# Performance work log

Hardware: AMD Instinct MI355X
Metric: run time of the kernel (lower is better)

The kernel has to match this reference:

```python
import jax, jax.numpy as jnp
import numpy as np

N_NODES = 10000
N_EDGES = 50000
UNITS = 64
NUM_GAUSSIANS = 50
MIN_D, MAX_D, GAMMA = 0.0, 30.0, 10.0


def setup_inputs() -> dict:
    key = jax.random.key(0)
    ks = jax.random.split(key, 8)
    node_features = jax.random.normal(ks[0], (N_NODES, UNITS), dtype=jnp.float32)
    edge_indices = jax.random.randint(ks[1], (2, N_EDGES), 0, N_NODES, dtype=jnp.int32)
    distances = jax.random.uniform(ks[2], (N_EDGES,), dtype=jnp.float32) * MAX_D
    # filter network params (Dense(units) -> Dense(units*units)), glorot-ish scales
    W1 = jax.random.normal(ks[3], (NUM_GAUSSIANS, UNITS), dtype=jnp.float32) * 0.13
    b1 = jnp.zeros((UNITS,), dtype=jnp.float32)
    W2 = jax.random.normal(ks[4], (UNITS, UNITS * UNITS), dtype=jnp.float32) * 0.02
    b2 = jnp.zeros((UNITS * UNITS,), dtype=jnp.float32)
    # transform Dense(units, use_bias=False)
    Wt = jax.random.normal(ks[5], (UNITS, UNITS), dtype=jnp.float32) * 0.125
    return {"node_features": node_features, "edge_indices": edge_indices,
            "distances": distances, "W1": W1, "b1": b1, "W2": W2, "b2": b2, "Wt": Wt}


def reference(node_features, edge_indices, distances, W1, b1, W2, b2, Wt):
    # Gaussian basis expansion: [E, G]
    centers = jnp.linspace(MIN_D, MAX_D, NUM_GAUSSIANS, dtype=jnp.float32)
    dist_feat = jnp.exp(-GAMMA * jnp.square(distances[:, None] - centers[None, :]))
    # filter-generating network -> per-edge [E, U, U] filters
    h = dist_feat @ W1 + b1
    filters = (h @ W2 + b2).reshape(-1, UNITS, UNITS)
    # gather source node feats, linear transform, per-edge matvec
    src = node_features[edge_indices[0]]            # [E, U]
    transformed = src @ Wt                          # [E, U]
    filtered = jnp.einsum('eij,ej->ei', filters, transformed)  # [E, U]
    # scatter-sum to destination nodes
    messages = jax.ops.segment_sum(filtered, edge_indices[1], num_segments=N_NODES)
    # shifted softplus: f(0) = 0
    return jax.nn.softplus(messages) - jnp.log(jnp.float32(2.0))
```

## Files before the change

### kernel.cpp

```cpp
#include <hip/hip_runtime.h>
#include <stdint.h>

#define UNITS 64
#define UU 4096
#define NG 50
#define NSLOT 51
#define GAMMA_C 10.0f
#define STEP_C (30.0f / 49.0f)
#define NWIN 4
#define NBKT 47

typedef __attribute__((ext_vector_type(8))) short bf16x8;
typedef __attribute__((ext_vector_type(4))) float f32x4;

__device__ __forceinline__ float bfu(uint16_t v) { return __uint_as_float(((uint32_t)v) << 16); }
__device__ __forceinline__ uint16_t f2bf(float x) {
  uint32_t u = __float_as_uint(x);
  u += 0x7fffu + ((u >> 16) & 1u);
  return (uint16_t)(u >> 16);
}
__device__ __forceinline__ uint32_t pk_bf16(float lo, float hi) {
  uint32_t r;
  asm("v_cvt_pk_bf16_f32 %0, %1, %2" : "=v"(r) : "v"(lo), "v"(hi));
  return r;
}
__device__ __forceinline__ int lo_of(float d) {
  int lo = (int)floorf(d * (1.0f / STEP_C)) - 1;
  return min(max(lo, 0), NG - NWIN);
}

__global__ void __launch_bounds__(256) k_at(
    const float* __restrict__ W1, const float* __restrict__ b1,
    const float* __restrict__ W2, const float* __restrict__ b2,
    const float* __restrict__ Wt, const float* __restrict__ dist,
    uint16_t* __restrict__ T5B, float* __restrict__ msg,
    int* __restrict__ bins, int* __restrict__ eidx,
    int n_out, int E, int ne) {
  int g = blockIdx.y, bx = blockIdx.x;
  if (g >= NSLOT) {
    if (g < NSLOT + 8) {
      int n4 = n_out >> 2;
      float4 z = {0.f, 0.f, 0.f, 0.f};
      for (int t = ((g - NSLOT) * 16 + bx) * 256 + threadIdx.x; t < n4; t += 128 * 256)
        reinterpret_cast<float4*>(msg)[t] = z;
    } else {
      __shared__ int hloc[NBKT];
      for (int i = threadIdx.x; i < NBKT; i += 256) hloc[i] = 0;
      __syncthreads();
      int tt = bx * 256 + threadIdx.x;
      for (int e = tt; e < E; e += 4096)
        atomicAdd(&hloc[lo_of(dist[e])], 1);
      __syncthreads();
      for (int i = threadIdx.x; i < NBKT; i += 256)
        if (hloc[i]) atomicAdd(&bins[i], hloc[i]);
      for (int i = tt; i < ne; i += 4096) eidx[i] = -1;
    }
    return;
  }
  __shared__ float Aloc[256];
  __shared__ float WtL[64 * 65];
  const int t = threadIdx.x;
  const int ij = bx * 256 + t;

  #pragma unroll
  for (int q = 0; q < 4; ++q) {
    int idx = q * 256 + t;
    float4 v = reinterpret_cast<const float4*>(Wt)[idx];
    int mm = idx >> 4, jj = (idx & 15) * 4;
    float* dst = &WtL[mm * 65 + jj];
    dst[0] = v.x; dst[1] = v.y; dst[2] = v.z; dst[3] = v.w;
  }
  {
    float acc = 0.f;
    if (g < NG) {
      const float* w1r = W1 + g * UNITS;
      #pragma unroll 8
      for (int k = 0; k < UNITS; ++k) acc = fmaf(w1r[k], W2[k * UU + ij], acc);
    } else {
      #pragma unroll 8
      for (int k = 0; k < UNITS; ++k) acc = fmaf(b1[k], W2[k * UU + ij], acc);
      acc += b2[ij];
    }
    Aloc[t] = acc;
  }
  __syncthreads();

  const int i_local = t >> 6, m = t & 63;
  const float* ar = &Aloc[i_local * 64];
  const float* wr = &WtL[m * 65];
  float acc = 0.f;
  #pragma unroll 8
  for (int j = 0; j < UNITS; ++j) acc = fmaf(ar[j], wr[j], acc);
  const int gi = bx * 4 + i_local;
  T5B[(((g << 3) + (m >> 3)) << 9) + (gi << 3) + (m & 7)] = f2bf(acc);
}

__global__ void k_scan(const int* __restrict__ bins, int* __restrict__ base,
                       int* __restrict__ cursor) {
  int l = threadIdx.x;
  int v = (l < NBKT) ? ((bins[l] + 15) >> 4) << 4 : 0;
  int inc = v;
  #pragma unroll
  for (int s = 1; s < 64; s <<= 1) {
    int t = __shfl_up(inc, s, 64);
    if (l >= s) inc += t;
  }
  int exc = inc - v;
  if (l < NBKT) { base[l] = exc; cursor[l] = exc; }
  if (l == NBKT) base[NBKT] = exc;
}

__global__ void __launch_bounds__(256) k_scat(const float* __restrict__ dist,
                                              int* __restrict__ cursor,
                                              int* __restrict__ eidx, int E) {
  __shared__ int hcnt[NBKT], hbase[NBKT], hcur[NBKT];
  int per = (E + gridDim.x - 1) / gridDim.x;
  int e0 = blockIdx.x * per, e1 = min(e0 + per, E);
  for (int i = threadIdx.x; i < NBKT; i += 256) { hcnt[i] = 0; hcur[i] = 0; }
  __syncthreads();
  for (int e = e0 + threadIdx.x; e < e1; e += 256)
    atomicAdd(&hcnt[lo_of(dist[e])], 1);
  __syncthreads();
  for (int i = threadIdx.x; i < NBKT; i += 256)
    hbase[i] = hcnt[i] ? atomicAdd(&cursor[i], hcnt[i]) : 0;
  __syncthreads();
  for (int e = e0 + threadIdx.x; e < e1; e += 256) {
    int b = lo_of(dist[e]);
    int p = hbase[b] + atomicAdd(&hcur[b], 1);
    eidx[p] = e;
  }
}

__global__ void __launch_bounds__(256) k_em(
    const float* __restrict__ nf, const int* __restrict__ ei,
    const float* __restrict__ dist, const uint16_t* __restrict__ T5B,
    const int* __restrict__ eidx, const int* __restrict__ base,
    float* __restrict__ msg, int E) {
  __shared__ float tile[4][16 * 64];
  int w = threadIdx.x >> 6, l = threadIdx.x & 63;
  int lr = l & 15, lg = l >> 4;
  int t16 = (blockIdx.x * 4 + w) * 16;
  int total = base[NBKT];
  if (t16 >= total) return;

  int b = 0;
  #pragma unroll
  for (int i = 1; i < NBKT; ++i) b += (t16 >= base[i]);

  int e = eidx[t16 + lr];
  bool valid = (e >= 0);
  int src = valid ? ei[e] : 0;
  int dst = valid ? ei[E + e] : -1;
  float d = valid ? dist[e] : 3.0e30f;

  float df[5];
  #pragma unroll
  for (int s = 0; s < NWIN; ++s) {
    float tt = d - (float)(b + s) * STEP_C;
    df[s] = __expf(-GAMMA_C * tt * tt);
  }
  df[NWIN] = valid ? 1.f : 0.f;

  union { bf16x8 v; uint32_t u[4]; } afr[2];
  const float4* ab = reinterpret_cast<const float4*>(nf + src * UNITS) + lg * 2;
  #pragma unroll
  for (int kk = 0; kk < 2; ++kk) {
    float4 v0 = ab[kk * 8], v1 = ab[kk * 8 + 1];
    afr[kk].u[0] = pk_bf16(v0.x, v0.y);
    afr[kk].u[1] = pk_bf16(v0.z, v0.w);
    afr[kk].u[2] = pk_bf16(v1.x, v1.y);
    afr[kk].u[3] = pk_bf16(v1.z, v1.w);
  }

  f32x4 run[4] = {};
  #pragma unroll
  for (int s = 0; s < 5; ++s) {
    int g = (s < NWIN) ? (b + s) : NG;
    const char* bb = (const char*)T5B + (g << 13) + (lg << 10) + (lr << 6);
    f32x4 acc[4] = {};
    #pragma unroll
    for (int kk = 0; kk < 2; ++kk)
      #pragma unroll
      for (int nt = 0; nt < 4; ++nt) {
        bf16x8 bf = *reinterpret_cast<const bf16x8*>(bb + (kk << 12) + (nt << 4));
        acc[nt] = __builtin_amdgcn_mfma_f32_16x16x32_bf16(afr[kk].v, bf, acc[nt], 0, 0, 0);
      }
    float dfq[4];
    #pragma unroll
    for (int q = 0; q < 4; ++q) dfq[q] = __shfl(df[s], lg * 4 + q, 64);
    #pragma unroll
    for (int nt = 0; nt < 4; ++nt)
      #pragma unroll
      for (int q = 0; q < 4; ++q)
        run[nt][q] = fmaf(dfq[q], acc[nt][q], run[nt][q]);
  }

  float* tw = tile[w];
  #pragma unroll
  for (int q = 0; q < 4; ++q) {
    float4 v4 = {run[0][q], run[1][q], run[2][q], run[3][q]};
    *reinterpret_cast<float4*>(&tw[(lg * 4 + q) * 64 + 4 * lr]) = v4;
  }
  asm volatile("" ::: "memory");

  #pragma unroll
  for (int r = 0; r < 16; ++r) {
    int dr = __shfl(dst, r, 64);
    if (dr < 0) continue;
    atomicAdd(&msg[dr * UNITS + l], tw[r * 64 + l]);
  }
}

__global__ void k_final(const float* __restrict__ msg, float* __restrict__ out, int n) {
  int i = blockIdx.x * 256 + threadIdx.x;
  if (i >= n) return;
  float x = msg[i];
  float sp = (x > 0.f) ? (x + log1pf(__expf(-x))) : log1pf(__expf(x));
  out[i] = sp - 0.69314718056f;
}

extern "C" void kernel_launch(void* const* d_in, const int* in_sizes, int n_in,
                              void* d_out, int out_size, void* d_ws, size_t ws_size,
                              hipStream_t stream) {
  const float* nf   = (const float*)d_in[0];
  const int*   ei   = (const int*)d_in[1];
  const float* dist = (const float*)d_in[2];
  const float* W1   = (const float*)d_in[3];
  const float* b1   = (const float*)d_in[4];
  const float* W2   = (const float*)d_in[5];
  const float* b2   = (const float*)d_in[6];
  const float* Wt   = (const float*)d_in[7];
  float* out = (float*)d_out;

  int E = in_sizes[2];
  int n_out = out_size;

  int mt = E / 16 + NBKT + 1;
  int ne = mt * 16;

  char* ws = (char*)d_ws;
  size_t off_msg  = 417792;
  size_t off_bins = off_msg + (size_t)n_out * 4;
  size_t off_base = off_bins + 64 * 4;
  size_t off_cur  = off_base + 64 * 4;
  size_t off_eidx = off_cur + 64 * 4;

  uint16_t* T5B   = (uint16_t*)ws;
  float*    msg   = (float*)(ws + off_msg);
  int*      bins  = (int*)(ws + off_bins);
  int*      base  = (int*)(ws + off_base);
  int*      cursor= (int*)(ws + off_cur);
  int*      eidx  = (int*)(ws + off_eidx);

  hipMemsetAsync(bins, 0, 64 * 4, stream);

  k_at  <<<dim3(16, NSLOT + 9), 256, 0, stream>>>(W1, b1, W2, b2, Wt, dist,
                                                  T5B, msg, bins, eidx, n_out, E, ne);
  k_scan<<<1, 64, 0, stream>>>(bins, base, cursor);
  k_scat<<<64, 256, 0, stream>>>(dist, cursor, eidx, E);
  k_em  <<<(mt + 3) / 4, 256, 0, stream>>>(nf, ei, dist, T5B, eidx, base, msg, E);
  k_final<<<(n_out + 255) / 256, 256, 0, stream>>>(msg, out, n_out);
}
```

Measured before the change: 48.20 us.

## Restructure bucketing pipeline to fold scan and scatter into other kernels

Histogramming moves into its own small kernel that runs first. The per-block prefix scan and the bucket scatter are folded into extra blocks of k_at, and k_em recomputes tile bases from the bin counts with a wave scan and ballot. This removes the separate k_scan and k_scat launches. The final softplus kernel is also vectorised to float4. The cost is redundant scan work in every block and scatter blocks that compete with the filter-precompute blocks.

```diff
diff --git a/kernel.cpp b/kernel.cpp
--- a/kernel.cpp
+++ b/kernel.cpp
@@ -13,7 +13,6 @@
 typedef __attribute__((ext_vector_type(8))) short bf16x8;
 typedef __attribute__((ext_vector_type(4))) float f32x4;
 
-__device__ __forceinline__ float bfu(uint16_t v) { return __uint_as_float(((uint32_t)v) << 16); }
 __device__ __forceinline__ uint16_t f2bf(float x) {
   uint32_t u = __float_as_uint(x);
   u += 0x7fffu + ((u >> 16) & 1u);
@@ -27,6 +26,21 @@
 __device__ __forceinline__ int lo_of(float d) {
   int lo = (int)floorf(d * (1.0f / STEP_C)) - 1;
   return min(max(lo, 0), NG - NWIN);
+}
+
+__global__ void __launch_bounds__(256) k_hist(const float* __restrict__ dist,
+                                              int* __restrict__ bins,
+                                              int* __restrict__ eidx, int E, int ne) {
+  __shared__ int hloc[NBKT];
+  for (int i = threadIdx.x; i < NBKT; i += 256) hloc[i] = 0;
+  __syncthreads();
+  int tt = blockIdx.x * 256 + threadIdx.x;
+  for (int e = tt; e < E; e += 64 * 256)
+    atomicAdd(&hloc[lo_of(dist[e])], 1);
+  __syncthreads();
+  for (int i = threadIdx.x; i < NBKT; i += 256)
+    if (hloc[i]) atomicAdd(&bins[i], hloc[i]);
+  for (int i = tt; i < ne; i += 64 * 256) eidx[i] = -1;
 }
 
 __global__ void __launch_bounds__(256) k_at(
@@ -34,8 +48,8 @@
     const float* __restrict__ W2, const float* __restrict__ b2,
     const float* __restrict__ Wt, const float* __restrict__ dist,
     uint16_t* __restrict__ T5B, float* __restrict__ msg,
-    int* __restrict__ bins, int* __restrict__ eidx,
-    int n_out, int E, int ne) {
+    const int* __restrict__ bins, int* __restrict__ rsv, int* __restrict__ eidx,
+    int n_out, int E) {
   int g = blockIdx.y, bx = blockIdx.x;
   if (g >= NSLOT) {
     if (g < NSLOT + 8) {
@@ -43,17 +57,36 @@
       float4 z = {0.f, 0.f, 0.f, 0.f};
       for (int t = ((g - NSLOT) * 16 + bx) * 256 + threadIdx.x; t < n4; t += 128 * 256)
         reinterpret_cast<float4*>(msg)[t] = z;
-    } else {
-      __shared__ int hloc[NBKT];
-      for (int i = threadIdx.x; i < NBKT; i += 256) hloc[i] = 0;
-      __syncthreads();
-      int tt = bx * 256 + threadIdx.x;
-      for (int e = tt; e < E; e += 4096)
-        atomicAdd(&hloc[lo_of(dist[e])], 1);
-      __syncthreads();
-      for (int i = threadIdx.x; i < NBKT; i += 256)
-        if (hloc[i]) atomicAdd(&bins[i], hloc[i]);
-      for (int i = tt; i < ne; i += 4096) eidx[i] = -1;
+      return;
+    }
+    __shared__ int sbase[NBKT];
+    __shared__ int hcnt[NBKT], hbase[NBKT], hcur[NBKT];
+    int sb = (g - (NSLOT + 8)) * 16 + bx;
+    int per = (E + 63) >> 6;
+    int e0 = sb * per, e1 = min(e0 + per, E);
+    if (threadIdx.x < 64) {
+      int lane = threadIdx.x;
+      int cap = (lane < NBKT) ? ((bins[lane] + 15) & ~15) : 0;
+      int inc = cap;
+      #pragma unroll
+      for (int s = 1; s < 64; s <<= 1) {
+        int t = __shfl_up(inc, s, 64);
+        if (lane >= s) inc += t;
+      }
+      if (lane < NBKT) sbase[lane] = inc - cap;
+    }
+    for (int i = threadIdx.x; i < NBKT; i += 256) { hcnt[i] = 0; hcur[i] = 0; }
+    __syncthreads();
+    for (int e = e0 + threadIdx.x; e < e1; e += 256)
+      atomicAdd(&hcnt[lo_of(dist[e])], 1);
+    __syncthreads();
+    for (int i = threadIdx.x; i < NBKT; i += 256)
+      hbase[i] = hcnt[i] ? (sbase[i] + atomicAdd(&rsv[i], hcnt[i])) : 0;
+    __syncthreads();
+    for (int e = e0 + threadIdx.x; e < e1; e += 256) {
+      int b = lo_of(dist[e]);
+      int p = hbase[b] + atomicAdd(&hcur[b], 1);
+      eidx[p] = e;
     }
     return;
   }
@@ -95,59 +128,33 @@
   T5B[(((g << 3) + (m >> 3)) << 9) + (gi << 3) + (m & 7)] = f2bf(acc);
 }
 
-__global__ void k_scan(const int* __restrict__ bins, int* __restrict__ base,
-                       int* __restrict__ cursor) {
-  int l = threadIdx.x;
-  int v = (l < NBKT) ? ((bins[l] + 15) >> 4) << 4 : 0;
-  int inc = v;
-  #pragma unroll
-  for (int s = 1; s < 64; s <<= 1) {
-    int t = __shfl_up(inc, s, 64);
-    if (l >= s) inc += t;
-  }
-  int exc = inc - v;
-  if (l < NBKT) { base[l] = exc; cursor[l] = exc; }
-  if (l == NBKT) base[NBKT] = exc;
-}
-
-__global__ void __launch_bounds__(256) k_scat(const float* __restrict__ dist,
-                                              int* __restrict__ cursor,
-                                              int* __restrict__ eidx, int E) {
-  __shared__ int hcnt[NBKT], hbase[NBKT], hcur[NBKT];
-  int per = (E + gridDim.x - 1) / gridDim.x;
-  int e0 = blockIdx.x * per, e1 = min(e0 + per, E);
-  for (int i = threadIdx.x; i < NBKT; i += 256) { hcnt[i] = 0; hcur[i] = 0; }
-  __syncthreads();
-  for (int e = e0 + threadIdx.x; e < e1; e += 256)
-    atomicAdd(&hcnt[lo_of(dist[e])], 1);
-  __syncthreads();
-  for (int i = threadIdx.x; i < NBKT; i += 256)
-    hbase[i] = hcnt[i] ? atomicAdd(&cursor[i], hcnt[i]) : 0;
-  __syncthreads();
-  for (int e = e0 + threadIdx.x; e < e1; e += 256) {
-    int b = lo_of(dist[e]);
-    int p = hbase[b] + atomicAdd(&hcur[b], 1);
-    eidx[p] = e;
-  }
-}
-
 __global__ void __launch_bounds__(256) k_em(
     const float* __restrict__ nf, const int* __restrict__ ei,
     const float* __restrict__ dist, const uint16_t* __restrict__ T5B,
-    const int* __restrict__ eidx, const int* __restrict__ base,
+    const int* __restrict__ eidx, const int* __restrict__ bins,
     float* __restrict__ msg, int E) {
   __shared__ float tile[4][16 * 64];
   int w = threadIdx.x >> 6, l = threadIdx.x & 63;
   int lr = l & 15, lg = l >> 4;
-  int t16 = (blockIdx.x * 4 + w) * 16;
-  int total = base[NBKT];
-  if (t16 >= total) return;
-
-  int b = 0;
-  #pragma unroll
-  for (int i = 1; i < NBKT; ++i) b += (t16 >= base[i]);
-
-  int e = eidx[t16 + lr];
+  int tileW = blockIdx.x * 4 + w;
+
+  int c = (l < NBKT) ? bins[l] : 0;
+  int tcap = (c + 15) >> 4;
+  int p = tcap;
+  #pragma unroll
+  for (int s = 1; s < 64; s <<= 1) {
+    int tt = __shfl_up(p, s, 64);
+    if (l >= s) p += tt;
+  }
+  int total = __shfl(p, 63);
+  if (tileW >= total) return;
+
+  uint64_t mb = __ballot(tileW < p);
+  int b = __ffsll((unsigned long long)mb) - 1;
+  int pb = __shfl(p, b), tb = __shfl(tcap, b);
+  int lt = tileW - (pb - tb);
+
+  int e = eidx[(pb - tb + lt) * 16 + lr];
   bool valid = (e >= 0);
   int src = valid ? ei[e] : 0;
   int dst = valid ? ei[E + e] : -1;
@@ -211,12 +218,17 @@
   }
 }
 
-__global__ void k_final(const float* __restrict__ msg, float* __restrict__ out, int n) {
-  int i = blockIdx.x * 256 + threadIdx.x;
-  if (i >= n) return;
-  float x = msg[i];
-  float sp = (x > 0.f) ? (x + log1pf(__expf(-x))) : log1pf(__expf(x));
-  out[i] = sp - 0.69314718056f;
+__global__ void k_final(const float* __restrict__ msg, float* __restrict__ out,
+                        int n_out) {
+  int i4 = blockIdx.x * 256 + threadIdx.x;
+  if (i4 >= (n_out >> 2)) return;
+  float4 a = reinterpret_cast<const float4*>(msg)[i4];
+  float4 r;
+  r.x = ((a.x > 0.f) ? (a.x + log1pf(__expf(-a.x))) : log1pf(__expf(a.x))) - 0.69314718056f;
+  r.y = ((a.y > 0.f) ? (a.y + log1pf(__expf(-a.y))) : log1pf(__expf(a.y))) - 0.69314718056f;
+  r.z = ((a.z > 0.f) ? (a.z + log1pf(__expf(-a.z))) : log1pf(__expf(a.z))) - 0.69314718056f;
+  r.w = ((a.w > 0.f) ? (a.w + log1pf(__expf(-a.w))) : log1pf(__expf(a.w))) - 0.69314718056f;
+  reinterpret_cast<float4*>(out)[i4] = r;
 }
 
 extern "C" void kernel_launch(void* const* d_in, const int* in_sizes, int n_in,
@@ -241,23 +253,20 @@
   char* ws = (char*)d_ws;
   size_t off_msg  = 417792;
   size_t off_bins = off_msg + (size_t)n_out * 4;
-  size_t off_base = off_bins + 64 * 4;
-  size_t off_cur  = off_base + 64 * 4;
-  size_t off_eidx = off_cur + 64 * 4;
-
-  uint16_t* T5B   = (uint16_t*)ws;
-  float*    msg   = (float*)(ws + off_msg);
-  int*      bins  = (int*)(ws + off_bins);
-  int*      base  = (int*)(ws + off_base);
-  int*      cursor= (int*)(ws + off_cur);
-  int*      eidx  = (int*)(ws + off_eidx);
-
-  hipMemsetAsync(bins, 0, 64 * 4, stream);
-
-  k_at  <<<dim3(16, NSLOT + 9), 256, 0, stream>>>(W1, b1, W2, b2, Wt, dist,
-                                                  T5B, msg, bins, eidx, n_out, E, ne);
-  k_scan<<<1, 64, 0, stream>>>(bins, base, cursor);
-  k_scat<<<64, 256, 0, stream>>>(dist, cursor, eidx, E);
-  k_em  <<<(mt + 3) / 4, 256, 0, stream>>>(nf, ei, dist, T5B, eidx, base, msg, E);
-  k_final<<<(n_out + 255) / 256, 256, 0, stream>>>(msg, out, n_out);
-}
+  size_t off_rsv  = off_bins + 64 * 4;
+  size_t off_eidx = off_rsv + 64 * 4;
+
+  uint16_t* T5B  = (uint16_t*)ws;
+  float*    msg  = (float*)(ws + off_msg);
+  int*      bins = (int*)(ws + off_bins);
+  int*      rsv  = (int*)(ws + off_rsv);
+  int*      eidx = (int*)(ws + off_eidx);
+
+  hipMemsetAsync(bins, 0, 128 * 4, stream);
+
+  k_hist<<<64, 256, 0, stream>>>(dist, bins, eidx, E, ne);
+  k_at  <<<dim3(16, NSLOT + 12), 256, 0, stream>>>(W1, b1, W2, b2, Wt, dist,
+                                                   T5B, msg, bins, rsv, eidx, n_out, E);
+  k_em  <<<(mt + 3) / 4, 256, 0, stream>>>(nf, ei, dist, T5B, eidx, bins, msg, E);
+  k_final<<<((n_out >> 2) + 255) / 256, 256, 0, stream>>>(msg, out, n_out);
+}
```

Result: faster. 44.92 us (-6.8%).
